# Optimization experiments

Hardware: AMD Instinct MI355X
Metric: run time of the kernel (lower is better)

The kernel has to match this reference:

```python
import jax, jax.numpy as jnp
import numpy as np

NBACTIONS = 4
TOTALNBINPUTS = 17  # RFSIZE*RFSIZE + ADDINPUT + NBACTIONS = 9 + 4 + 4
H = 4096


def setup_inputs() -> dict:
    key = jax.random.key(0)
    ks = jax.random.split(key, 12)
    x = jax.random.normal(ks[0], (1, TOTALNBINPUTS), dtype=jnp.float32)
    hidden = 0.1 * jax.random.normal(ks[1], (1, H), dtype=jnp.float32)
    hebb = 0.01 * jax.random.normal(ks[2], (H, H), dtype=jnp.float32)
    # i2h Linear(17 -> H); store weight as [in, out]
    Wi = jax.random.normal(ks[3], (TOTALNBINPUTS, H), dtype=jnp.float32) / np.sqrt(TOTALNBINPUTS)
    bi = jax.random.normal(ks[4], (H,), dtype=jnp.float32) * 0.01
    # plastic recurrent params (0.01 * rand, as in torch init)
    w = 0.01 * jax.random.uniform(ks[5], (H, H), dtype=jnp.float32)
    alpha = 0.01 * jax.random.uniform(ks[6], (H, H), dtype=jnp.float32)
    eta = jnp.full((1,), 0.01, dtype=jnp.float32)
    # heads
    Wo = jax.random.normal(ks[7], (H, NBACTIONS), dtype=jnp.float32) / np.sqrt(H)
    bo = jax.random.normal(ks[8], (NBACTIONS,), dtype=jnp.float32) * 0.01
    Wv = jax.random.normal(ks[9], (H, 1), dtype=jnp.float32) / np.sqrt(H)
    bv = jax.random.normal(ks[10], (1,), dtype=jnp.float32) * 0.01
    return {"x": x, "hidden": hidden, "hebb": hebb, "Wi": Wi, "bi": bi,
            "w": w, "alpha": alpha, "eta": eta, "Wo": Wo, "bo": bo,
            "Wv": Wv, "bv": bv}


def reference(x, hidden, hebb, Wi, bi, w, alpha, eta, Wo, bo, Wv, bv):
    # type='plastic', rule='hebb', activ='tanh'
    # hactiv = tanh(i2h(x) + hidden @ (w + alpha * hebb))   [1, H]
    hactiv = jnp.tanh(x @ Wi + bi + hidden @ (w + alpha * hebb))
    # hebb <- (1 - eta) * hebb + eta * outer(hidden, hactiv)   [H, H]
    hebb_new = (1.0 - eta) * hebb + eta * jnp.outer(hidden[0], hactiv[0])
    activout = jax.nn.softmax(hactiv @ Wo + bo, axis=-1)  # [1, NBACTIONS]
    valueout = hactiv @ Wv + bv                            # [1, 1]
    return (activout, valueout, hactiv, hebb_new)
```

## Files before the change

kernel.cpp:

```cpp
#include <hip/hip_runtime.h>
#include <math.h>

#define H 4096
#define NIN 17
#define H4 (H / 4)
#define NSPLIT 512
#define ROWS_PER_SPLIT (H / NSPLIT)
#define NSPLIT2 32

#define OUT_HACTIV_OFF  5
#define OUT_HEBB_OFF    4101
#define OUT_PARTIAL_OFF 4104
#define OUT_PARTIAL2_OFF (OUT_PARTIAL_OFF + NSPLIT * H)

__global__ __launch_bounds__(256, 4) void kA(const float* __restrict__ hidden,
                                             const float* __restrict__ w,
                                             const float* __restrict__ alpha,
                                             const float* __restrict__ hebb,
                                             float* __restrict__ partial) {
    const int j4 = blockIdx.x * 256 + threadIdx.x;
    const int r0 = blockIdx.y * ROWS_PER_SPLIT;
    const float4* __restrict__ w4 = (const float4*)w;
    const float4* __restrict__ a4 = (const float4*)alpha;
    const float4* __restrict__ b4 = (const float4*)hebb;
    float4 acc = make_float4(0.f, 0.f, 0.f, 0.f);
#pragma unroll
    for (int r = 0; r < ROWS_PER_SPLIT; ++r) {
        const int i = r0 + r;
        const float hv = hidden[i];
        const int base = i * H4 + j4;
        const float4 wv = w4[base];
        const float4 av = a4[base];
        const float4 bv = b4[base];
        acc.x += hv * (wv.x + av.x * bv.x);
        acc.y += hv * (wv.y + av.y * bv.y);
        acc.z += hv * (wv.z + av.z * bv.z);
        acc.w += hv * (wv.w + av.w * bv.w);
    }
    ((float4*)partial)[blockIdx.y * H4 + j4] = acc;
}

__global__ __launch_bounds__(256) void kB1(const float* __restrict__ partial,
                                           float* __restrict__ partial2) {
    const int j4 = blockIdx.x * 256 + threadIdx.x;
    const float4* __restrict__ p4 = (const float4*)partial;
    float4 acc = make_float4(0.f, 0.f, 0.f, 0.f);
#pragma unroll
    for (int s = 0; s < NSPLIT / NSPLIT2; ++s) {
        const float4 v = p4[(blockIdx.y * (NSPLIT / NSPLIT2) + s) * H4 + j4];
        acc.x += v.x; acc.y += v.y; acc.z += v.z; acc.w += v.w;
    }
    ((float4*)partial2)[blockIdx.y * H4 + j4] = acc;
}

__global__ __launch_bounds__(256) void kB2(const float* __restrict__ x,
                                           const float* __restrict__ Wi,
                                           const float* __restrict__ bi,
                                           const float* __restrict__ partial2,
                                           float* __restrict__ hactiv) {
    const int j = blockIdx.x * 256 + threadIdx.x;
    float s = bi[j];
#pragma unroll
    for (int k = 0; k < NIN; ++k) s += x[k] * Wi[k * H + j];
#pragma unroll
    for (int sp = 0; sp < NSPLIT2; ++sp) s += partial2[sp * H + j];
    hactiv[j] = tanhf(s);
}

__global__ __launch_bounds__(256) void kC(const float* __restrict__ hebb,
                                          const float* __restrict__ hidden,
                                          const float* __restrict__ eta_p,
                                          const float* __restrict__ Wo,
                                          const float* __restrict__ bo,
                                          const float* __restrict__ Wv,
                                          const float* __restrict__ bv,
                                          float* __restrict__ out) {
    const float* __restrict__ hactiv = out + OUT_HACTIV_OFF;
    float* __restrict__ hebb_out = out + OUT_HEBB_OFF;
    const unsigned nHebbBlocks = (unsigned)(H * (H / 256));

    if (blockIdx.x < nHebbBlocks) {
        const unsigned g = blockIdx.x * 256u + threadIdx.x;
        const unsigned i = g >> 12;
        const unsigned col = g & (H - 1);
        const float eta = eta_p[0];
        hebb_out[g] = (1.f - eta) * hebb[g] + eta * hidden[i] * hactiv[col];
    } else {
        __shared__ float red[5][256];
        float a0 = 0.f, a1 = 0.f, a2 = 0.f, a3 = 0.f, av = 0.f;
        const float4* __restrict__ Wo4 = (const float4*)Wo;
        for (int i = threadIdx.x; i < H; i += 256) {
            const float h = hactiv[i];
            const float4 wo = Wo4[i];
            a0 += h * wo.x;
            a1 += h * wo.y;
            a2 += h * wo.z;
            a3 += h * wo.w;
            av += h * Wv[i];
        }
        red[0][threadIdx.x] = a0;
        red[1][threadIdx.x] = a1;
        red[2][threadIdx.x] = a2;
        red[3][threadIdx.x] = a3;
        red[4][threadIdx.x] = av;
        __syncthreads();
        for (int s = 128; s > 0; s >>= 1) {
            if ((int)threadIdx.x < s) {
#pragma unroll
                for (int k = 0; k < 5; ++k)
                    red[k][threadIdx.x] += red[k][threadIdx.x + s];
            }
            __syncthreads();
        }
        if (threadIdx.x == 0) {
            const float z0 = red[0][0] + bo[0];
            const float z1 = red[1][0] + bo[1];
            const float z2 = red[2][0] + bo[2];
            const float z3 = red[3][0] + bo[3];
            const float m = fmaxf(fmaxf(z0, z1), fmaxf(z2, z3));
            const float e0 = expf(z0 - m);
            const float e1 = expf(z1 - m);
            const float e2 = expf(z2 - m);
            const float e3 = expf(z3 - m);
            const float inv = 1.f / (e0 + e1 + e2 + e3);
            out[0] = e0 * inv;
            out[1] = e1 * inv;
            out[2] = e2 * inv;
            out[3] = e3 * inv;
            out[4] = red[4][0] + bv[0];
        }
    }
}

extern "C" void kernel_launch(void* const* d_in, const int* in_sizes, int n_in,
                              void* d_out, int out_size, void* d_ws, size_t ws_size,
                              hipStream_t stream) {
    const float* x      = (const float*)d_in[0];
    const float* hidden = (const float*)d_in[1];
    const float* hebb   = (const float*)d_in[2];
    const float* Wi     = (const float*)d_in[3];
    const float* bi     = (const float*)d_in[4];
    const float* w      = (const float*)d_in[5];
    const float* alpha  = (const float*)d_in[6];
    const float* eta    = (const float*)d_in[7];
    const float* Wo     = (const float*)d_in[8];
    const float* bo     = (const float*)d_in[9];
    const float* Wv     = (const float*)d_in[10];
    const float* bv     = (const float*)d_in[11];
    float* out = (float*)d_out;

    float* partial  = out + OUT_PARTIAL_OFF;
    float* partial2 = out + OUT_PARTIAL2_OFF;
    float* hactiv   = out + OUT_HACTIV_OFF;

    kA<<<dim3(4, NSPLIT), 256, 0, stream>>>(hidden, w, alpha, hebb, partial);
    kB1<<<dim3(4, NSPLIT2), 256, 0, stream>>>(partial, partial2);
    kB2<<<16, 256, 0, stream>>>(x, Wi, bi, partial2, hactiv);
    kC<<<65537, 256, 0, stream>>>(hebb, hidden, eta, Wo, bo, Wv, bv, out);
}
```

Measured before the change: 276.4 us.

## Widen kA per-thread work and use nontemporal loads/stores for streaming matrices

kA now launches one block per row split, and each thread accumulates four float4 columns across the full row width instead of one. The loads of w, alpha and hebb and the stores of the partial sums become nontemporal, as do the hebb read and hebb_out write in kC. The goal is to cut block-launch count and keep single-use streaming data from polluting the caches. The risk is that 512 blocks give lower occupancy under the relaxed launch bounds, and that kC's hebb reread can no longer hit in cache after kA.

```diff
diff --git a/kernel.cpp b/kernel.cpp
--- a/kernel.cpp
+++ b/kernel.cpp
@@ -8,49 +8,59 @@
 #define ROWS_PER_SPLIT (H / NSPLIT)
 #define NSPLIT2 32
 
+typedef float vf4 __attribute__((ext_vector_type(4)));
+
 #define OUT_HACTIV_OFF  5
 #define OUT_HEBB_OFF    4101
 #define OUT_PARTIAL_OFF 4104
 #define OUT_PARTIAL2_OFF (OUT_PARTIAL_OFF + NSPLIT * H)
 
-__global__ __launch_bounds__(256, 4) void kA(const float* __restrict__ hidden,
+__global__ __launch_bounds__(256, 2) void kA(const float* __restrict__ hidden,
                                              const float* __restrict__ w,
                                              const float* __restrict__ alpha,
                                              const float* __restrict__ hebb,
                                              float* __restrict__ partial) {
-    const int j4 = blockIdx.x * 256 + threadIdx.x;
-    const int r0 = blockIdx.y * ROWS_PER_SPLIT;
-    const float4* __restrict__ w4 = (const float4*)w;
-    const float4* __restrict__ a4 = (const float4*)alpha;
-    const float4* __restrict__ b4 = (const float4*)hebb;
-    float4 acc = make_float4(0.f, 0.f, 0.f, 0.f);
+    const int t = threadIdx.x;
+    const int b = blockIdx.x;
+    const int r0 = b * ROWS_PER_SPLIT;
+    const vf4* __restrict__ w4 = (const vf4*)w;
+    const vf4* __restrict__ a4 = (const vf4*)alpha;
+    const vf4* __restrict__ b4 = (const vf4*)hebb;
+
+    vf4 acc[4];
 #pragma unroll
+    for (int k = 0; k < 4; ++k) acc[k] = (vf4)(0.f);
+
+#pragma unroll 2
     for (int r = 0; r < ROWS_PER_SPLIT; ++r) {
         const int i = r0 + r;
         const float hv = hidden[i];
-        const int base = i * H4 + j4;
-        const float4 wv = w4[base];
-        const float4 av = a4[base];
-        const float4 bv = b4[base];
-        acc.x += hv * (wv.x + av.x * bv.x);
-        acc.y += hv * (wv.y + av.y * bv.y);
-        acc.z += hv * (wv.z + av.z * bv.z);
-        acc.w += hv * (wv.w + av.w * bv.w);
+        const int rowbase = i * H4;
+#pragma unroll
+        for (int k = 0; k < 4; ++k) {
+            const int idx = rowbase + t + k * 256;
+            const vf4 wv = __builtin_nontemporal_load(&w4[idx]);
+            const vf4 av = __builtin_nontemporal_load(&a4[idx]);
+            const vf4 bv = __builtin_nontemporal_load(&b4[idx]);
+            acc[k] += hv * (wv + av * bv);
+        }
     }
-    ((float4*)partial)[blockIdx.y * H4 + j4] = acc;
+    vf4* __restrict__ p4 = (vf4*)partial;
+#pragma unroll
+    for (int k = 0; k < 4; ++k)
+        __builtin_nontemporal_store(acc[k], &p4[(b << 10) + t + k * 256]);
 }
 
 __global__ __launch_bounds__(256) void kB1(const float* __restrict__ partial,
                                            float* __restrict__ partial2) {
     const int j4 = blockIdx.x * 256 + threadIdx.x;
-    const float4* __restrict__ p4 = (const float4*)partial;
-    float4 acc = make_float4(0.f, 0.f, 0.f, 0.f);
+    const vf4* __restrict__ p4 = (const vf4*)partial;
+    vf4 acc = (vf4)(0.f);
 #pragma unroll
     for (int s = 0; s < NSPLIT / NSPLIT2; ++s) {
-        const float4 v = p4[(blockIdx.y * (NSPLIT / NSPLIT2) + s) * H4 + j4];
-        acc.x += v.x; acc.y += v.y; acc.z += v.z; acc.w += v.w;
+        acc += p4[(blockIdx.y * (NSPLIT / NSPLIT2) + s) * H4 + j4];
     }
-    ((float4*)partial2)[blockIdx.y * H4 + j4] = acc;
+    ((vf4*)partial2)[blockIdx.y * H4 + j4] = acc;
 }
 
 __global__ __launch_bounds__(256) void kB2(const float* __restrict__ x,
@@ -84,14 +94,16 @@
         const unsigned i = g >> 12;
         const unsigned col = g & (H - 1);
         const float eta = eta_p[0];
-        hebb_out[g] = (1.f - eta) * hebb[g] + eta * hidden[i] * hactiv[col];
+        const float hv = __builtin_nontemporal_load(&hebb[g]);
+        const float v = (1.f - eta) * hv + eta * hidden[i] * hactiv[col];
+        __builtin_nontemporal_store(v, &hebb_out[g]);
     } else {
         __shared__ float red[5][256];
         float a0 = 0.f, a1 = 0.f, a2 = 0.f, a3 = 0.f, av = 0.f;
-        const float4* __restrict__ Wo4 = (const float4*)Wo;
+        const vf4* __restrict__ Wo4 = (const vf4*)Wo;
         for (int i = threadIdx.x; i < H; i += 256) {
             const float h = hactiv[i];
-            const float4 wo = Wo4[i];
+            const vf4 wo = Wo4[i];
             a0 += h * wo.x;
             a1 += h * wo.y;
             a2 += h * wo.z;
@@ -153,7 +165,7 @@
     float* partial2 = out + OUT_PARTIAL2_OFF;
     float* hactiv   = out + OUT_HACTIV_OFF;
 
-    kA<<<dim3(4, NSPLIT), 256, 0, stream>>>(hidden, w, alpha, hebb, partial);
+    kA<<<NSPLIT, 256, 0, stream>>>(hidden, w, alpha, hebb, partial);
     kB1<<<dim3(4, NSPLIT2), 256, 0, stream>>>(partial, partial2);
     kB2<<<16, 256, 0, stream>>>(x, Wi, bi, partial2, hactiv);
     kC<<<65537, 256, 0, stream>>>(hebb, hidden, eta, Wo, bo, Wv, bv, out);
```

Result: faster. 262.9 us (-4.9%).
